# Kernel optimization log

Hardware: AMD Instinct MI355X
Metric: run time of the kernel (lower is better)

## Reference

```python
import jax, jax.numpy as jnp
import numpy as np

N = 16384   # num nodes
E = 524288  # num edges (avg degree 32)
C = 128     # in_channels == hidden_channels (residual requires equality)


def setup_inputs() -> dict:
    key = jax.random.key(0)
    ks = jax.random.split(key, 16)
    s = 1.0 / np.sqrt(C)  # glorot-ish scale
    return {
        "x": jax.random.normal(ks[0], (N, C), dtype=jnp.float32),
        "edge_index": jax.random.randint(ks[1], (2, E), 0, N, dtype=jnp.int32),
        "edge_attr": jax.random.normal(ks[2], (E, 8), dtype=jnp.float32),
        # GATConv 1 params
        "W1": jax.random.normal(ks[3], (C, C), dtype=jnp.float32) * s,
        "a_src1": jax.random.normal(ks[4], (C,), dtype=jnp.float32) * s,
        "a_dst1": jax.random.normal(ks[5], (C,), dtype=jnp.float32) * s,
        "b1": jnp.zeros((C,), dtype=jnp.float32),
        # GATConv 2 params
        "W2": jax.random.normal(ks[6], (C, C), dtype=jnp.float32) * s,
        "a_src2": jax.random.normal(ks[7], (C,), dtype=jnp.float32) * s,
        "a_dst2": jax.random.normal(ks[8], (C,), dtype=jnp.float32) * s,
        "b2": jnp.zeros((C,), dtype=jnp.float32),
        # TemporalAttention params
        "att_weight": jax.random.normal(ks[9], (C, C), dtype=jnp.float32) * s,
        "att_bias": jnp.zeros((C,), dtype=jnp.float32),
        # LayerNorm params
        "ln_gamma": jnp.ones((C,), dtype=jnp.float32),
        "ln_beta": jnp.zeros((C,), dtype=jnp.float32),
    }


def _gat_conv(x, edge_index, W, a_src, a_dst, b):
    """PyG GATConv, heads=1, negative_slope=0.2, add_self_loops=True.
    Edge (j -> i): src = edge_index[0], dst = edge_index[1]; softmax over dst."""
    n = x.shape[0]
    xw = x @ W                                   # [N, C]
    loops = jnp.arange(n, dtype=edge_index.dtype)
    src = jnp.concatenate([edge_index[0], loops])  # [E+N]
    dst = jnp.concatenate([edge_index[1], loops])
    alpha_src = xw @ a_src                       # [N]
    alpha_dst = xw @ a_dst                       # [N]
    e = jax.nn.leaky_relu(alpha_src[src] + alpha_dst[dst], negative_slope=0.2)
    # numerically stable segment softmax over destination nodes
    e_max = jax.ops.segment_max(e, dst, num_segments=n)
    p = jnp.exp(e - e_max[dst])
    denom = jax.ops.segment_sum(p, dst, num_segments=n)
    alpha = p / denom[dst]                       # [E+N]
    out = jax.ops.segment_sum(alpha[:, None] * xw[src], dst, num_segments=n)
    return out + b


def reference(x, edge_index, edge_attr, W1, a_src1, a_dst1, b1,
              W2, a_src2, a_dst2, b2, att_weight, att_bias, ln_gamma, ln_beta):
    # edge_attr is accepted but unused: GATConv was built without edge_dim,
    # so PyG ignores it in the attention computation.
    h = jax.nn.relu(_gat_conv(x, edge_index, W1, a_src1, a_dst1, b1))
    # dropout p=0.2 is identity in eval mode
    h = _gat_conv(h, edge_index, W2, a_src2, a_dst2, b2)

    # TemporalAttention over the (batch=1, N, C) view -> dense NxN attention
    q = h @ att_weight                            # [N, C]
    scores = (q @ h.T) / jnp.sqrt(jnp.float32(h.shape[-1]))  # [N, N]
    attn = jax.nn.softmax(scores, axis=-1)
    h = attn @ h + att_bias                       # [N, C]

    h = h + x                                     # residual
    mu = jnp.mean(h, axis=-1, keepdims=True)
    var = jnp.var(h, axis=-1, keepdims=True)
    h = (h - mu) / jnp.sqrt(var + 1e-5) * ln_gamma + ln_beta
    return h
```

## Files before the change

kernel.cpp:

```cpp
#include <hip/hip_runtime.h>

#define CC 128

typedef __attribute__((ext_vector_type(8))) short bf16x8;
typedef __attribute__((ext_vector_type(16))) float f32x16;

static __device__ __forceinline__ float lrelu(float v){ return v > 0.f ? v : 0.2f*v; }
static __device__ __forceinline__ unsigned short f2bf(float f){
  unsigned u = __float_as_uint(f);
  unsigned r = (u + 0x7fffu + ((u >> 16) & 1u)) >> 16;
  return (unsigned short)r;
}
static __device__ __forceinline__ float bf2f(unsigned short s){
  return __uint_as_float(((unsigned)s) << 16);
}
static __device__ __forceinline__ unsigned cvtpk(float lo, float hi){
  unsigned r;
  asm("v_cvt_pk_bf16_f32 %0, %1, %2" : "=v"(r) : "v"(lo), "v"(hi));
  return r;
}

#define QSCALE (0.08838834764831845f * 1.4426950408889634f)
#define L2E 1.4426950408889634f

#if defined(__has_builtin)
#if __has_builtin(__builtin_amdgcn_global_load_lds)
#define HAVE_GLL 1
#endif
#endif

#ifdef HAVE_GLL
static __device__ __forceinline__ void gload_lds16(const uint4* g, uint4* l){
  __builtin_amdgcn_global_load_lds(
      (const __attribute__((address_space(1))) unsigned int*)(const void*)g,
      (__attribute__((address_space(3))) unsigned int*)(void*)l, 16, 0, 0);
}
#endif

__global__ __launch_bounds__(256) void pack_w3(const float* __restrict__ W1,
                                               const float* __restrict__ W2,
                                               const float* __restrict__ Wa,
                                               unsigned short* __restrict__ img){
  int gid = blockIdx.x*256 + threadIdx.x;
  int m = gid >> 11, u = gid & 2047;
  const float* W = (m==0) ? W1 : (m==1) ? W2 : Wa;
  int k = u >> 8, ct = (u >> 6) & 3, l = u & 63;
  int h = l >> 5, c = ct*32 + (l & 31);
  int k0 = k*16 + h*8;
  float f[8];
  #pragma unroll
  for (int j=0;j<8;j++) f[j] = W[(k0+j)*CC + c];
  uint4 o;
  o.x = cvtpk(f[0],f[1]); o.y = cvtpk(f[2],f[3]);
  o.z = cvtpk(f[4],f[5]); o.w = cvtpk(f[6],f[7]);
  *(uint4*)&img[((size_t)m*2048 + u)*8] = o;
}

template<bool ABF16, int OMODE>
__global__ __launch_bounds__(256) void gemm_mfma(const void* __restrict__ Av,
                                                 const uint4* __restrict__ Wimg,
                                                 unsigned short* __restrict__ out){
  __shared__ uint4 WS[2048];
  const int tid = threadIdx.x, lane = tid & 63, w = tid >> 6;
  const int h = lane >> 5, l31 = lane & 31;
  const long r0 = (long)blockIdx.x * 64;
#ifdef HAVE_GLL
  #pragma unroll
  for (int i=0;i<8;i++){ int u = i*256 + w*64; gload_lds16(Wimg + u + lane, &WS[u]); }
#else
  #pragma unroll
  for (int i=0;i<8;i++){ int u = i*256 + tid; WS[u] = Wimg[u]; }
#endif
  const int rt = w & 1, ct0 = (w >> 1) * 2;
  const long arow = (r0 + rt*32 + l31)*CC + h*8;
  f32x16 acc0 = {}, acc1 = {};
  __syncthreads();
  #pragma unroll
  for (int k=0;k<8;k++){
    bf16x8 afr;
    if (ABF16){
      afr = *(const bf16x8*)&((const unsigned short*)Av)[arow + k*16];
    } else {
      const float* ap = (const float*)Av + arow + k*16;
      float4 a0 = *(const float4*)ap;
      float4 a1 = *(const float4*)(ap+4);
      uint4 av;
      av.x = cvtpk(a0.x,a0.y); av.y = cvtpk(a0.z,a0.w);
      av.z = cvtpk(a1.x,a1.y); av.w = cvtpk(a1.z,a1.w);
      __builtin_memcpy(&afr, &av, 16);
    }
    bf16x8 b0 = *(const bf16x8*)&WS[(k*4+ct0  )*64 + lane];
    bf16x8 b1 = *(const bf16x8*)&WS[(k*4+ct0+1)*64 + lane];
    acc0 = __builtin_amdgcn_mfma_f32_32x32x16_bf16(afr, b0, acc0, 0,0,0);
    acc1 = __builtin_amdgcn_mfma_f32_32x32x16_bf16(afr, b1, acc1, 0,0,0);
  }
  #pragma unroll
  for (int r=0;r<16;r++){
    long row = r0 + rt*32 + (r&3) + 8*(r>>2) + 4*h;
    float s0 = (OMODE==1) ? acc0[r]*QSCALE : acc0[r];
    float s1 = (OMODE==1) ? acc1[r]*QSCALE : acc1[r];
    out[row*CC + ct0*32 + l31]     = f2bf(s0);
    out[row*CC + (ct0+1)*32 + l31] = f2bf(s1);
  }
}

__global__ __launch_bounds__(256) void rowdot2b(const unsigned short* __restrict__ X,
                                                const float* __restrict__ a1,
                                                const float* __restrict__ a2,
                                                float* __restrict__ as_, float* __restrict__ ad_){
  const int lane = threadIdx.x & 63;
  const long row = (long)blockIdx.x*4 + (threadIdx.x >> 6);
  unsigned u = *(const unsigned*)&X[row*CC + lane*2];
  float v0 = bf2f((unsigned short)(u & 0xffffu));
  float v1 = bf2f((unsigned short)(u >> 16));
  float2 w1 = ((const float2*)a1)[lane];
  float2 w2 = ((const float2*)a2)[lane];
  float s1 = v0*w1.x + v1*w1.y;
  float s2 = v0*w2.x + v1*w2.y;
  #pragma unroll
  for (int off=32; off; off>>=1){
    s1 += __shfl_xor(s1, off);
    s2 += __shfl_xor(s2, off);
  }
  if (lane==0){ as_[row]=s1; ad_[row]=s2; }
}

__global__ void zero_int(int* __restrict__ p, int n){
  int i = blockIdx.x*256 + threadIdx.x;
  if (i < n) p[i] = 0;
}
__global__ void csr_hist(const int* __restrict__ ei, int* __restrict__ deg, int E){
  int e = blockIdx.x*256 + threadIdx.x;
  if (e < E) atomicAdd(&deg[ei[E + e]], 1);
}
__global__ __launch_bounds__(256) void csr_scan(const int* __restrict__ deg,
                                                int* __restrict__ rowptr,
                                                int* __restrict__ cursor, int N){
  __shared__ int part[257];
  const int t = threadIdx.x;
  const int per = N / 256;
  const int base = t*per;
  int s = 0;
  for (int j=0;j<per;j++) s += deg[base+j];
  part[t+1] = s;
  if (t==0) part[0] = 0;
  __syncthreads();
  if (t==0){
    for (int i=1;i<=256;i++) part[i] += part[i-1];
  }
  __syncthreads();
  int run = part[t];
  for (int j=0;j<per;j++){
    rowptr[base+j] = run;
    cursor[base+j] = run;
    run += deg[base+j];
  }
  if (t==255) rowptr[N] = run;
}
__global__ void csr_fill(const int* __restrict__ ei, int* __restrict__ cursor,
                         int* __restrict__ csrc, int E){
  int e = blockIdx.x*256 + threadIdx.x;
  if (e < E){
    int d = ei[E + e];
    int slot = atomicAdd(&cursor[d], 1);
    csrc[slot] = ei[e];
  }
}

template<bool RELUOUT>
__global__ __launch_bounds__(256) void gat_gather(
    const int* __restrict__ rowptr, const int* __restrict__ csrc,
    const float* __restrict__ as_, const float* __restrict__ ad_,
    const unsigned short* __restrict__ X, const float* __restrict__ b,
    unsigned short* __restrict__ O, int N){
  const int lane = threadIdx.x & 63;
  const int half = lane >> 5, l32 = lane & 31;
  const int dst = blockIdx.x*4 + (threadIdx.x >> 6);
  const float adv = ad_[dst];
  float m = lrelu(as_[dst] + adv);
  float l = 1.f;
  float acc0=0.f, acc1=0.f, acc2=0.f, acc3=0.f;
  if (half == 0){
    ushort4 v = *(const ushort4*)&X[(size_t)dst*CC + l32*4];
    acc0 = bf2f(v.x); acc1 = bf2f(v.y); acc2 = bf2f(v.z); acc3 = bf2f(v.w);
  }
  const int kb = rowptr[dst];
  const int deg = rowptr[dst+1] - kb;
  for (int c0 = 0; c0 < deg; c0 += 64){
    const int nv = min(64, deg - c0);
    int src = dst; float e = -3.0e38f;
    if (lane < nv){
      src = csrc[kb + c0 + lane];
      e = lrelu(as_[src] + adv);
    }
    float cm = e;
    #pragma unroll
    for (int off=32; off; off>>=1) cm = fmaxf(cm, __shfl_xor(cm, off));
    if (cm > m){
      float fr = __builtin_amdgcn_exp2f((m - cm)*L2E);
      l *= fr; acc0 *= fr; acc1 *= fr; acc2 *= fr; acc3 *= fr;
      m = cm;
    }
    float p = __builtin_amdgcn_exp2f((e - m)*L2E);
    float cs = p;
    #pragma unroll
    for (int off=32; off; off>>=1) cs += __shfl_xor(cs, off);
    l += cs;
    for (int j = 0; j < nv; j += 2){
      float w0 = __shfl(p, j);
      float w1 = __shfl(p, (j+1)&63);
      w1 = (j+1 < nv) ? w1 : 0.f;
      int s0 = __shfl(src, j);
      int s1 = __shfl(src, (j+1)&63);
      float wgt = half ? w1 : w0;
      int s = half ? s1 : s0;
      ushort4 v = *(const ushort4*)&X[(size_t)s*CC + l32*4];
      acc0 += wgt*bf2f(v.x); acc1 += wgt*bf2f(v.y);
      acc2 += wgt*bf2f(v.z); acc3 += wgt*bf2f(v.w);
    }
  }
  acc0 += __shfl_xor(acc0, 32);
  acc1 += __shfl_xor(acc1, 32);
  acc2 += __shfl_xor(acc2, 32);
  acc3 += __shfl_xor(acc3, 32);
  if (half == 0){
    float inv = 1.f / l;
    float4 bb = *(const float4*)&b[l32*4];
    float r0 = acc0*inv + bb.x, r1 = acc1*inv + bb.y;
    float r2 = acc2*inv + bb.z, r3 = acc3*inv + bb.w;
    if (RELUOUT){
      r0=fmaxf(r0,0.f); r1=fmaxf(r1,0.f); r2=fmaxf(r2,0.f); r3=fmaxf(r3,0.f);
    }
    uint2 o; o.x = cvtpk(r0,r1); o.y = cvtpk(r2,r3);
    *(uint2*)&O[(size_t)dst*CC + l32*4] = o;
  }
}

template<int NKT>
__global__ __launch_bounds__(256) void convert_pack(const unsigned short* __restrict__ h,
                                                    uint4* __restrict__ IMG, int N){
  const int KVB = NKT*32;
  int idx = blockIdx.x*256 + threadIdx.x;
  int tile = idx / (NKT*1024);
  int u = idx - tile*(NKT*1024);
  int l = u & 63, hh = l >> 5, l31 = l & 31;
  if (u < NKT*512){
    int kt = u >> 9, ks = (u >> 6) & 7;
    int key = tile*KVB + kt*32 + l31;
    IMG[idx] = *(const uint4*)&h[(size_t)key*CC + ks*16 + hh*8];
  } else {
    int v = u - NKT*512;
    int ks = (v >> 6) & (2*NKT - 1);
    int ct = v >> (NKT==1 ? 7 : 8);
    int c = ct*32 + l31;
    int key0 = tile*KVB + ks*16 + hh*8;
    unsigned short o[8];
    #pragma unroll
    for (int j=0;j<8;j++) o[j] = h[(size_t)(key0+j)*CC + c];
    IMG[idx] = *(uint4*)o;
  }
}

template<int NKT>
__global__ __launch_bounds__(256,2) void attn_mfma(
    const unsigned short* __restrict__ Qb, const uint4* __restrict__ IMG,
    unsigned short* __restrict__ opW, float* __restrict__ ml, int N, int nsplit){
  const int TILE4 = NKT*1024;
  __shared__ uint4 SH[2*NKT*1024];

  const int tid = threadIdx.x;
  const int lane = tid & 63, w = tid >> 6;
  const int h = lane >> 5, q31 = lane & 31;
  const int flat = blockIdx.x;
  const int split = flat % nsplit;
  const int qb0 = (flat / nsplit) * 128;
  const int KVB = NKT*32;
  const int ntt = N / KVB;
  const int tb = (ntt*split)/nsplit, te = (ntt*(split+1))/nsplit;

  bf16x8 qf[8];
  const int qrow = qb0 + w*32 + q31;
  #pragma unroll
  for (int ks=0; ks<8; ks++)
    qf[ks] = *(const bf16x8*)&Qb[(size_t)qrow*CC + ks*16 + h*8];

  f32x16 acc_o[4] = {};
  float m_ = -3.0e38f, l_ = 0.f;

  int cur = 0;
  {
    const uint4* src = IMG + (size_t)tb*TILE4;
#ifdef HAVE_GLL
    #pragma unroll
    for (int i=0;i<NKT*4;i++){ int u = i*256 + w*64; gload_lds16(src + u + lane, &SH[u]); }
#else
    #pragma unroll
    for (int i=0;i<NKT*4;i++){ int u = i*256 + tid; SH[u] = src[u]; }
#endif
  }

  for (int t=tb; t<te; t++){
    __syncthreads();
    if (t+1 < te){
      const uint4* src = IMG + (size_t)(t+1)*TILE4;
      uint4* dst = &SH[(cur^1)*TILE4];
#ifdef HAVE_GLL
      #pragma unroll
      for (int i=0;i<NKT*4;i++){ int u = i*256 + w*64; gload_lds16(src + u + lane, dst + u); }
#else
      #pragma unroll
      for (int i=0;i<NKT*4;i++){ int u = i*256 + tid; dst[u] = src[u]; }
#endif
    }
    const uint4* B = &SH[cur*TILE4];

    f32x16 accs[NKT];
    #pragma unroll
    for (int kt=0; kt<NKT; kt++){
      f32x16 a = {};
      __builtin_amdgcn_s_setprio(1);
      #pragma unroll
      for (int ks=0; ks<8; ks++){
        bf16x8 hf = *(const bf16x8*)&B[(kt*8+ks)*64 + lane];
        a = __builtin_amdgcn_mfma_f32_32x32x16_bf16(hf, qf[ks], a, 0,0,0);
      }
      __builtin_amdgcn_s_setprio(0);
      accs[kt] = a;
    }

    float tmax[16];
    #pragma unroll
    for (int r=0;r<16;r++){
      float v = accs[0][r];
      if (NKT == 2) v = fmaxf(v, accs[1][r]);
      tmax[r] = v;
    }
    #pragma unroll
    for (int s=8; s; s>>=1)
      #pragma unroll
      for (int r=0;r<s;r++) tmax[r] = fmaxf(tmax[r], tmax[r+s]);
    float tm = fmaxf(tmax[0], __shfl_xor(tmax[0], 32));
    if (!__all(tm <= m_ + 11.0f)){
      float mn = fmaxf(m_, tm);
      float fr = __builtin_amdgcn_exp2f(m_ - mn);
      m_ = mn; l_ *= fr;
      #pragma unroll
      for (int ct=0; ct<4; ct++)
        #pragma unroll
        for (int r=0;r<16;r++) acc_o[ct][r] *= fr;
    }
    float psum[16];
    #pragma unroll
    for (int kt=0; kt<NKT; kt++)
      #pragma unroll
      for (int r=0;r<16;r++)
        accs[kt][r] = __builtin_amdgcn_exp2f(accs[kt][r] - m_);
    #pragma unroll
    for (int r=0;r<16;r++){
      float v = accs[0][r];
      if (NKT == 2) v += accs[1][r];
      psum[r] = v;
    }
    #pragma unroll
    for (int s=8; s; s>>=1)
      #pragma unroll
      for (int r=0;r<s;r++) psum[r] += psum[r+s];
    l_ += psum[0] + __shfl_xor(psum[0], 32);

    unsigned pk[NKT][8];
    #pragma unroll
    for (int kt=0; kt<NKT; kt++)
      #pragma unroll
      for (int wd=0; wd<8; wd++)
        pk[kt][wd] = cvtpk(accs[kt][2*wd], accs[kt][2*wd+1]);

    #pragma unroll
    for (int ks=0; ks<2*NKT; ks++){
      const int kt = ks >> 1, W = (ks & 1)*4;
      unsigned w0o = pk[kt][W+0], w1o = pk[kt][W+1];
      unsigned w2o = pk[kt][W+2], w3o = pk[kt][W+3];
      unsigned va = h ? w0o : w2o;
      unsigned vb = h ? w1o : w3o;
      unsigned fa = (unsigned)__shfl_xor((int)va, 32);
      unsigned fb = (unsigned)__shfl_xor((int)vb, 32);
      uint4 fw;
      fw.x = h ? fa : w0o;
      fw.y = h ? fb : w1o;
      fw.z = h ? w2o : fa;
      fw.w = h ? w3o : fb;
      bf16x8 pfrag;
      __builtin_memcpy(&pfrag, &fw, 16);
      __builtin_amdgcn_s_setprio(1);
      #pragma unroll
      for (int ct=0; ct<4; ct++){
        bf16x8 hf = *(const bf16x8*)&B[NKT*512 + (ct*2*NKT+ks)*64 + lane];
        acc_o[ct] = __builtin_amdgcn_mfma_f32_32x32x16_bf16(hf, pfrag, acc_o[ct], 0,0,0);
      }
      __builtin_amdgcn_s_setprio(0);
    }
    cur ^= 1;
  }

  float inv = 1.f / l_;
  unsigned apk[4][8];
  #pragma unroll
  for (int ct=0; ct<4; ct++)
    #pragma unroll
    for (int wd=0; wd<8; wd++)
      apk[ct][wd] = cvtpk(acc_o[ct][2*wd]*inv, acc_o[ct][2*wd+1]*inv);

  unsigned short* orow = opW + (size_t)split*N*CC + (size_t)qrow*CC + h*64;
  #pragma unroll
  for (int cp=0; cp<2; cp++){
    #pragma unroll
    for (int jp=0; jp<4; jp++){
      int wd0 = 2*jp, wd1 = 2*jp+1;
      unsigned a0 = apk[cp][wd0],   a1 = apk[cp][wd1];
      unsigned b0 = apk[cp+2][wd0], b1 = apk[cp+2][wd1];
      unsigned v0 = h ? a0 : b0;
      unsigned v1 = h ? a1 : b1;
      unsigned f0 = (unsigned)__shfl_xor((int)v0, 32);
      unsigned f1 = (unsigned)__shfl_xor((int)v1, 32);
      unsigned o0 = h ? b0 : a0;
      unsigned o1 = h ? b1 : a1;
      uint4 st;
      st.x = h ? f0 : o0;
      st.y = h ? f1 : o1;
      st.z = h ? o0 : f0;
      st.w = h ? o1 : f1;
      *(uint4*)&orow[cp*32 + jp*8] = st;
    }
  }
  if (lane < 32)
    ((float2*)ml)[(size_t)split*N + qrow] = make_float2(m_, l_);
}

template<int NS>
__global__ __launch_bounds__(256) void merge_ln(
    const unsigned short* __restrict__ opW, const float* __restrict__ ml,
    const float* __restrict__ x, const float* __restrict__ ab,
    const float* __restrict__ gam, const float* __restrict__ bet,
    float* __restrict__ out, int N){
  const int lane = threadIdx.x & 63;
  const long row = (long)blockIdx.x*4 + (threadIdx.x >> 6);
  float mm[NS], ll[NS];
  float M = -3.0e38f;
  #pragma unroll
  for (int i=0;i<NS;i++){
    float2 v = ((const float2*)ml)[(size_t)i*N + row];
    mm[i]=v.x; ll[i]=v.y;
    M = fmaxf(M, v.x);
  }
  float den = 0.f;
  float wgt[NS];
  #pragma unroll
  for (int i=0;i<NS;i++){ wgt[i] = exp2f(mm[i]-M)*ll[i]; den += wgt[i]; }
  float invd = 1.f/den;
  float o0 = 0.f, o1 = 0.f;
  #pragma unroll
  for (int i=0;i<NS;i++){
    unsigned u = *(const unsigned*)&opW[((size_t)i*N + row)*CC + lane*2];
    float c = wgt[i]*invd;
    o0 += c * bf2f((unsigned short)(u & 0xffffu));
    o1 += c * bf2f((unsigned short)(u >> 16));
  }
  float2 xb = ((const float2*)(x + row*CC))[lane];
  float2 bb = ((const float2*)ab)[lane];
  float a0 = o0 + bb.x + xb.x;
  float a1 = o1 + bb.y + xb.y;
  float s = a0 + a1, ss = a0*a0 + a1*a1;
  #pragma unroll
  for (int off=32; off; off>>=1){ s += __shfl_xor(s,off); ss += __shfl_xor(ss,off); }
  float mu  = s * (1.f/128.f);
  float var = ss * (1.f/128.f) - mu*mu;
  float rstd = rsqrtf(var + 1e-5f);
  float2 gg = ((const float2*)gam)[lane];
  float2 b2 = ((const float2*)bet)[lane];
  float2 r;
  r.x = (a0 - mu)*rstd*gg.x + b2.x;
  r.y = (a1 - mu)*rstd*gg.y + b2.y;
  ((float2*)(out + row*CC))[lane] = r;
}

extern "C" void kernel_launch(void* const* d_in, const int* in_sizes, int n_in,
                              void* d_out, int out_size, void* d_ws, size_t ws_size,
                              hipStream_t stream) {
  const float* x   = (const float*)d_in[0];
  const int*   ei  = (const int*)d_in[1];
  const float* W1  = (const float*)d_in[3];
  const float* a_s1= (const float*)d_in[4];
  const float* a_d1= (const float*)d_in[5];
  const float* b1  = (const float*)d_in[6];
  const float* W2  = (const float*)d_in[7];
  const float* a_s2= (const float*)d_in[8];
  const float* a_d2= (const float*)d_in[9];
  const float* b2  = (const float*)d_in[10];
  const float* Wa  = (const float*)d_in[11];
  const float* ab  = (const float*)d_in[12];
  const float* g   = (const float*)d_in[13];
  const float* be  = (const float*)d_in[14];
  float* out = (float*)d_out;

  const int N = in_sizes[0] / CC;
  const int E = in_sizes[1] / 2;
  const size_t MB = 1024*1024;
  const size_t KB = 1024;

  char* base = (char*)d_ws;
  uint4* IMG  = (uint4*)(base);
  unsigned short* xwb = (unsigned short*)(base + 8*MB);
  unsigned short* hW  = (unsigned short*)(base + 12*MB);
  int* csrc   = (int*)(base + 16*MB);
  int* rowptr = (int*)(base + 18*MB);
  int* cursor = (int*)(base + 18*MB + 128*KB);
  int* deg    = (int*)(base + 18*MB + 256*KB);
  float* as_  = (float*)(base + 18*MB + 384*KB);
  float* ad_  = (float*)(base + 18*MB + 512*KB);
  unsigned short* Wimg = (unsigned short*)(base + 19*MB);
  unsigned short* opW  = (unsigned short*)(base + 8*MB);
  unsigned short* QbD  = (unsigned short*)d_out;

  const uint4* W1i = (const uint4*)(Wimg);
  const uint4* W2i = (const uint4*)(Wimg + 2048*8);
  const uint4* Wai = (const uint4*)(Wimg + 2*2048*8);

  const bool big = (ws_size >= 41*MB);
  const int ns = big ? 8 : 4;
  float* ml = (float*)(base + 8*MB + (size_t)ns*4*MB);

  dim3 B(256);

  pack_w3<<<24, B, 0, stream>>>(W1, W2, Wa, Wimg);
  zero_int<<<(N+255)/256, B, 0, stream>>>(deg, N);
  csr_hist<<<(E+255)/256, B, 0, stream>>>(ei, deg, E);
  csr_scan<<<1, B, 0, stream>>>(deg, rowptr, cursor, N);
  csr_fill<<<(E+255)/256, B, 0, stream>>>(ei, cursor, csrc, E);

  gemm_mfma<false,0><<<N/64, B, 0, stream>>>(x, W1i, xwb);
  rowdot2b<<<N/4, B, 0, stream>>>(xwb, a_s1, a_d1, as_, ad_);
  gat_gather<true><<<N/4, B, 0, stream>>>(rowptr, csrc, as_, ad_, xwb, b1, hW, N);

  gemm_mfma<true,0><<<N/64, B, 0, stream>>>(hW, W2i, xwb);
  rowdot2b<<<N/4, B, 0, stream>>>(xwb, a_s2, a_d2, as_, ad_);
  gat_gather<false><<<N/4, B, 0, stream>>>(rowptr, csrc, as_, ad_, xwb, b2, hW, N);

  gemm_mfma<true,1><<<N/64, B, 0, stream>>>(hW, Wai, QbD);
  if (big){
    convert_pack<1><<<(N*32)/256, B, 0, stream>>>(hW, IMG, N);
    attn_mfma<1><<<(N/128)*8, B, 0, stream>>>(QbD, IMG, opW, ml, N, 8);
    merge_ln<8><<<N/4, B, 0, stream>>>(opW, ml, x, ab, g, be, out, N);
  } else {
    convert_pack<2><<<(N*32)/256, B, 0, stream>>>(hW, IMG, N);
    attn_mfma<2><<<(N/128)*4, B, 0, stream>>>(QbD, IMG, opW, ml, N, 4);
    merge_ln<4><<<N/4, B, 0, stream>>>(opW, ml, x, ab, g, be, out, N);
  }
}
```

Before: 332.5 us.

## Process two query tiles per wave in attention kernel to reuse K/V fragments

Each wave in the flash-attention kernel now handles NQT query tiles of 32 rows. Every K/V fragment loaded from LDS feeds NQT MFMAs instead of one. The big path uses NQT=2 with half as many blocks, so LDS traffic and tile loads per query drop. The cost is doubled accumulator and Q-fragment registers, which may cause spills or lower occupancy under launch_bounds(256,2), and fewer blocks are available to fill the GPU.

After: 321.0 us. 3.4% less time.

```diff
diff --git a/kernel.cpp b/kernel.cpp
--- a/kernel.cpp
+++ b/kernel.cpp
@@ -261,7 +261,7 @@
   }
 }
 
-template<int NKT>
+template<int NKT, int NQT>
 __global__ __launch_bounds__(256,2) void attn_mfma(
     const unsigned short* __restrict__ Qb, const uint4* __restrict__ IMG,
     unsigned short* __restrict__ opW, float* __restrict__ ml, int N, int nsplit){
@@ -273,19 +273,30 @@
   const int h = lane >> 5, q31 = lane & 31;
   const int flat = blockIdx.x;
   const int split = flat % nsplit;
-  const int qb0 = (flat / nsplit) * 128;
+  const int qb0 = (flat / nsplit) * (128*NQT);
   const int KVB = NKT*32;
   const int ntt = N / KVB;
   const int tb = (ntt*split)/nsplit, te = (ntt*(split+1))/nsplit;
 
-  bf16x8 qf[8];
-  const int qrow = qb0 + w*32 + q31;
-  #pragma unroll
-  for (int ks=0; ks<8; ks++)
-    qf[ks] = *(const bf16x8*)&Qb[(size_t)qrow*CC + ks*16 + h*8];
-
-  f32x16 acc_o[4] = {};
-  float m_ = -3.0e38f, l_ = 0.f;
+  int qrow[NQT];
+  bf16x8 qf[NQT][8];
+  #pragma unroll
+  for (int qt=0; qt<NQT; qt++){
+    qrow[qt] = qb0 + w*(32*NQT) + qt*32 + q31;
+    #pragma unroll
+    for (int ks=0; ks<8; ks++)
+      qf[qt][ks] = *(const bf16x8*)&Qb[(size_t)qrow[qt]*CC + ks*16 + h*8];
+  }
+
+  f32x16 zero16 = {};
+  f32x16 acc_o[4][NQT];
+  #pragma unroll
+  for (int ct=0; ct<4; ct++)
+    #pragma unroll
+    for (int qt=0; qt<NQT; qt++) acc_o[ct][qt] = zero16;
+  float m_[NQT], l_[NQT];
+  #pragma unroll
+  for (int qt=0; qt<NQT; qt++){ m_[qt] = -3.0e38f; l_[qt] = 0.f; }
 
   int cur = 0;
   {
@@ -314,125 +325,147 @@
     }
     const uint4* B = &SH[cur*TILE4];
 
-    f32x16 accs[NKT];
+    f32x16 accs[NKT][NQT];
     #pragma unroll
     for (int kt=0; kt<NKT; kt++){
-      f32x16 a = {};
+      #pragma unroll
+      for (int qt=0; qt<NQT; qt++) accs[kt][qt] = zero16;
       __builtin_amdgcn_s_setprio(1);
       #pragma unroll
       for (int ks=0; ks<8; ks++){
         bf16x8 hf = *(const bf16x8*)&B[(kt*8+ks)*64 + lane];
-        a = __builtin_amdgcn_mfma_f32_32x32x16_bf16(hf, qf[ks], a, 0,0,0);
+        #pragma unroll
+        for (int qt=0; qt<NQT; qt++)
+          accs[kt][qt] = __builtin_amdgcn_mfma_f32_32x32x16_bf16(hf, qf[qt][ks], accs[kt][qt], 0,0,0);
       }
       __builtin_amdgcn_s_setprio(0);
-      accs[kt] = a;
-    }
-
-    float tmax[16];
-    #pragma unroll
-    for (int r=0;r<16;r++){
-      float v = accs[0][r];
-      if (NKT == 2) v = fmaxf(v, accs[1][r]);
-      tmax[r] = v;
-    }
-    #pragma unroll
-    for (int s=8; s; s>>=1)
-      #pragma unroll
-      for (int r=0;r<s;r++) tmax[r] = fmaxf(tmax[r], tmax[r+s]);
-    float tm = fmaxf(tmax[0], __shfl_xor(tmax[0], 32));
-    if (!__all(tm <= m_ + 11.0f)){
-      float mn = fmaxf(m_, tm);
-      float fr = __builtin_amdgcn_exp2f(m_ - mn);
-      m_ = mn; l_ *= fr;
-      #pragma unroll
-      for (int ct=0; ct<4; ct++)
-        #pragma unroll
-        for (int r=0;r<16;r++) acc_o[ct][r] *= fr;
-    }
-    float psum[16];
-    #pragma unroll
-    for (int kt=0; kt<NKT; kt++)
-      #pragma unroll
-      for (int r=0;r<16;r++)
-        accs[kt][r] = __builtin_amdgcn_exp2f(accs[kt][r] - m_);
-    #pragma unroll
-    for (int r=0;r<16;r++){
-      float v = accs[0][r];
-      if (NKT == 2) v += accs[1][r];
-      psum[r] = v;
-    }
-    #pragma unroll
-    for (int s=8; s; s>>=1)
-      #pragma unroll
-      for (int r=0;r<s;r++) psum[r] += psum[r+s];
-    l_ += psum[0] + __shfl_xor(psum[0], 32);
-
-    unsigned pk[NKT][8];
-    #pragma unroll
-    for (int kt=0; kt<NKT; kt++)
-      #pragma unroll
-      for (int wd=0; wd<8; wd++)
-        pk[kt][wd] = cvtpk(accs[kt][2*wd], accs[kt][2*wd+1]);
+    }
+
+    float tm[NQT];
+    #pragma unroll
+    for (int qt=0; qt<NQT; qt++){
+      float tmax[16];
+      #pragma unroll
+      for (int r=0;r<16;r++){
+        float v = accs[0][qt][r];
+        if (NKT == 2) v = fmaxf(v, accs[1][qt][r]);
+        tmax[r] = v;
+      }
+      #pragma unroll
+      for (int s=8; s; s>>=1)
+        #pragma unroll
+        for (int r=0;r<s;r++) tmax[r] = fmaxf(tmax[r], tmax[r+s]);
+      tm[qt] = fmaxf(tmax[0], __shfl_xor(tmax[0], 32));
+    }
+    bool ok = true;
+    #pragma unroll
+    for (int qt=0; qt<NQT; qt++) ok &= (tm[qt] <= m_[qt] + 11.0f);
+    if (!__all(ok)){
+      #pragma unroll
+      for (int qt=0; qt<NQT; qt++){
+        float mn = fmaxf(m_[qt], tm[qt]);
+        float fr = __builtin_amdgcn_exp2f(m_[qt] - mn);
+        m_[qt] = mn; l_[qt] *= fr;
+        #pragma unroll
+        for (int ct=0; ct<4; ct++)
+          #pragma unroll
+          for (int r=0;r<16;r++) acc_o[ct][qt][r] *= fr;
+      }
+    }
+    unsigned pk[NQT][NKT][8];
+    #pragma unroll
+    for (int qt=0; qt<NQT; qt++){
+      float psum[16];
+      #pragma unroll
+      for (int kt=0; kt<NKT; kt++)
+        #pragma unroll
+        for (int r=0;r<16;r++)
+          accs[kt][qt][r] = __builtin_amdgcn_exp2f(accs[kt][qt][r] - m_[qt]);
+      #pragma unroll
+      for (int r=0;r<16;r++){
+        float v = accs[0][qt][r];
+        if (NKT == 2) v += accs[1][qt][r];
+        psum[r] = v;
+      }
+      #pragma unroll
+      for (int s=8; s; s>>=1)
+        #pragma unroll
+        for (int r=0;r<s;r++) psum[r] += psum[r+s];
+      l_[qt] += psum[0] + __shfl_xor(psum[0], 32);
+      #pragma unroll
+      for (int kt=0; kt<NKT; kt++)
+        #pragma unroll
+        for (int wd=0; wd<8; wd++)
+          pk[qt][kt][wd] = cvtpk(accs[kt][qt][2*wd], accs[kt][qt][2*wd+1]);
+    }
 
     #pragma unroll
     for (int ks=0; ks<2*NKT; ks++){
       const int kt = ks >> 1, W = (ks & 1)*4;
-      unsigned w0o = pk[kt][W+0], w1o = pk[kt][W+1];
-      unsigned w2o = pk[kt][W+2], w3o = pk[kt][W+3];
-      unsigned va = h ? w0o : w2o;
-      unsigned vb = h ? w1o : w3o;
-      unsigned fa = (unsigned)__shfl_xor((int)va, 32);
-      unsigned fb = (unsigned)__shfl_xor((int)vb, 32);
-      uint4 fw;
-      fw.x = h ? fa : w0o;
-      fw.y = h ? fb : w1o;
-      fw.z = h ? w2o : fa;
-      fw.w = h ? w3o : fb;
-      bf16x8 pfrag;
-      __builtin_memcpy(&pfrag, &fw, 16);
+      bf16x8 pfrag[NQT];
+      #pragma unroll
+      for (int qt=0; qt<NQT; qt++){
+        unsigned w0o = pk[qt][kt][W+0], w1o = pk[qt][kt][W+1];
+        unsigned w2o = pk[qt][kt][W+2], w3o = pk[qt][kt][W+3];
+        unsigned va = h ? w0o : w2o;
+        unsigned vb = h ? w1o : w3o;
+        unsigned fa = (unsigned)__shfl_xor((int)va, 32);
+        unsigned fb = (unsigned)__shfl_xor((int)vb, 32);
+        uint4 fw;
+        fw.x = h ? fa : w0o;
+        fw.y = h ? fb : w1o;
+        fw.z = h ? w2o : fa;
+        fw.w = h ? w3o : fb;
+        __builtin_memcpy(&pfrag[qt], &fw, 16);
+      }
       __builtin_amdgcn_s_setprio(1);
       #pragma unroll
       for (int ct=0; ct<4; ct++){
         bf16x8 hf = *(const bf16x8*)&B[NKT*512 + (ct*2*NKT+ks)*64 + lane];
-        acc_o[ct] = __builtin_amdgcn_mfma_f32_32x32x16_bf16(hf, pfrag, acc_o[ct], 0,0,0);
+        #pragma unroll
+        for (int qt=0; qt<NQT; qt++)
+          acc_o[ct][qt] = __builtin_amdgcn_mfma_f32_32x32x16_bf16(hf, pfrag[qt], acc_o[ct][qt], 0,0,0);
       }
       __builtin_amdgcn_s_setprio(0);
     }
     cur ^= 1;
   }
 
-  float inv = 1.f / l_;
-  unsigned apk[4][8];
-  #pragma unroll
-  for (int ct=0; ct<4; ct++)
-    #pragma unroll
-    for (int wd=0; wd<8; wd++)
-      apk[ct][wd] = cvtpk(acc_o[ct][2*wd]*inv, acc_o[ct][2*wd+1]*inv);
-
-  unsigned short* orow = opW + (size_t)split*N*CC + (size_t)qrow*CC + h*64;
-  #pragma unroll
-  for (int cp=0; cp<2; cp++){
-    #pragma unroll
-    for (int jp=0; jp<4; jp++){
-      int wd0 = 2*jp, wd1 = 2*jp+1;
-      unsigned a0 = apk[cp][wd0],   a1 = apk[cp][wd1];
-      unsigned b0 = apk[cp+2][wd0], b1 = apk[cp+2][wd1];
-      unsigned v0 = h ? a0 : b0;
-      unsigned v1 = h ? a1 : b1;
-      unsigned f0 = (unsigned)__shfl_xor((int)v0, 32);
-      unsigned f1 = (unsigned)__shfl_xor((int)v1, 32);
-      unsigned o0 = h ? b0 : a0;
-      unsigned o1 = h ? b1 : a1;
-      uint4 st;
-      st.x = h ? f0 : o0;
-      st.y = h ? f1 : o1;
-      st.z = h ? o0 : f0;
-      st.w = h ? o1 : f1;
-      *(uint4*)&orow[cp*32 + jp*8] = st;
-    }
-  }
-  if (lane < 32)
-    ((float2*)ml)[(size_t)split*N + qrow] = make_float2(m_, l_);
+  #pragma unroll
+  for (int qt=0; qt<NQT; qt++){
+    float inv = 1.f / l_[qt];
+    unsigned apk[4][8];
+    #pragma unroll
+    for (int ct=0; ct<4; ct++)
+      #pragma unroll
+      for (int wd=0; wd<8; wd++)
+        apk[ct][wd] = cvtpk(acc_o[ct][qt][2*wd]*inv, acc_o[ct][qt][2*wd+1]*inv);
+
+    unsigned short* orow = opW + (size_t)split*N*CC + (size_t)qrow[qt]*CC + h*64;
+    #pragma unroll
+    for (int cp=0; cp<2; cp++){
+      #pragma unroll
+      for (int jp=0; jp<4; jp++){
+        int wd0 = 2*jp, wd1 = 2*jp+1;
+        unsigned a0 = apk[cp][wd0],   a1 = apk[cp][wd1];
+        unsigned b0 = apk[cp+2][wd0], b1 = apk[cp+2][wd1];
+        unsigned v0 = h ? a0 : b0;
+        unsigned v1 = h ? a1 : b1;
+        unsigned f0 = (unsigned)__shfl_xor((int)v0, 32);
+        unsigned f1 = (unsigned)__shfl_xor((int)v1, 32);
+        unsigned o0 = h ? b0 : a0;
+        unsigned o1 = h ? b1 : a1;
+        uint4 st;
+        st.x = h ? f0 : o0;
+        st.y = h ? f1 : o1;
+        st.z = h ? o0 : f0;
+        st.w = h ? o1 : f1;
+        *(uint4*)&orow[cp*32 + jp*8] = st;
+      }
+    }
+    if (lane < 32)
+      ((float2*)ml)[(size_t)split*N + qrow[qt]] = make_float2(m_[qt], l_[qt]);
+  }
 }
 
 template<int NS>
@@ -547,11 +580,11 @@
   gemm_mfma<true,1><<<N/64, B, 0, stream>>>(hW, Wai, QbD);
   if (big){
     convert_pack<1><<<(N*32)/256, B, 0, stream>>>(hW, IMG, N);
-    attn_mfma<1><<<(N/128)*8, B, 0, stream>>>(QbD, IMG, opW, ml, N, 8);
+    attn_mfma<1,2><<<(N/256)*8, B, 0, stream>>>(QbD, IMG, opW, ml, N, 8);
     merge_ln<8><<<N/4, B, 0, stream>>>(opW, ml, x, ab, g, be, out, N);
   } else {
     convert_pack<2><<<(N*32)/256, B, 0, stream>>>(hW, IMG, N);
-    attn_mfma<2><<<(N/128)*4, B, 0, stream>>>(QbD, IMG, opW, ml, N, 4);
+    attn_mfma<2,1><<<(N/128)*4, B, 0, stream>>>(QbD, IMG, opW, ml, N, 4);
     merge_ln<4><<<N/4, B, 0, stream>>>(opW, ml, x, ab, g, be, out, N);
   }
 }
```

## Software-pipeline flash attention with triple-buffered tiles overlapping QK and PV

Applied to the files above, without the earlier changes.

Replaces the double-buffered attention kernel with one that stages 32-key tiles into three LDS buffers. It issues the QK^T MFMAs for the next tile while the current tile's softmax and PV product run. The aim is to hide the softmax's exp/reduction latency and the tile loads behind matrix-core work. The tile size is fixed at 32 keys for all sizes, and the loop is unrolled by two, which assumes an even tile count per split. Register pressure rises because two score tiles are live at once, and the setprio hints are dropped.

Result: no change. 336.1 us (+1.1%).

```diff
diff --git a/kernel.cpp b/kernel.cpp
--- a/kernel.cpp
+++ b/kernel.cpp
@@ -236,24 +236,22 @@
   }
 }
 
-template<int NKT>
 __global__ __launch_bounds__(256) void convert_pack(const unsigned short* __restrict__ h,
                                                     uint4* __restrict__ IMG, int N){
-  const int KVB = NKT*32;
   int idx = blockIdx.x*256 + threadIdx.x;
-  int tile = idx / (NKT*1024);
-  int u = idx - tile*(NKT*1024);
+  int tile = idx >> 10;
+  int u = idx & 1023;
   int l = u & 63, hh = l >> 5, l31 = l & 31;
-  if (u < NKT*512){
-    int kt = u >> 9, ks = (u >> 6) & 7;
-    int key = tile*KVB + kt*32 + l31;
+  if (u < 512){
+    int ks = u >> 6;
+    int key = tile*32 + l31;
     IMG[idx] = *(const uint4*)&h[(size_t)key*CC + ks*16 + hh*8];
   } else {
-    int v = u - NKT*512;
-    int ks = (v >> 6) & (2*NKT - 1);
-    int ct = v >> (NKT==1 ? 7 : 8);
+    int v = u - 512;
+    int ks = (v >> 6) & 1;
+    int ct = v >> 7;
     int c = ct*32 + l31;
-    int key0 = tile*KVB + ks*16 + hh*8;
+    int key0 = tile*32 + ks*16 + hh*8;
     unsigned short o[8];
     #pragma unroll
     for (int j=0;j<8;j++) o[j] = h[(size_t)(key0+j)*CC + c];
@@ -261,12 +259,89 @@
   }
 }
 
-template<int NKT>
-__global__ __launch_bounds__(256,2) void attn_mfma(
+static __device__ __forceinline__ void stage_tile(uint4* dst, const uint4* src, int w, int lane){
+#ifdef HAVE_GLL
+  #pragma unroll
+  for (int i=0;i<4;i++) gload_lds16(src + i*256 + w*64 + lane, dst + i*256 + w*64);
+#else
+  int tid = w*64 + lane;
+  #pragma unroll
+  for (int i=0;i<4;i++) dst[i*256 + tid] = src[i*256 + tid];
+#endif
+}
+
+static __device__ __forceinline__ f32x16 sphase(const uint4* buf, const bf16x8 (&qf)[8], int lane){
+  f32x16 a = {};
+  #pragma unroll
+  for (int ks=0; ks<8; ks++){
+    bf16x8 hf = *(const bf16x8*)&buf[ks*64 + lane];
+    a = __builtin_amdgcn_mfma_f32_32x32x16_bf16(hf, qf[ks], a, 0,0,0);
+  }
+  return a;
+}
+
+static __device__ __forceinline__ void softmax_pk(f32x16& s, float& m_, float& l_,
+                                                  f32x16 (&acc_o)[4], unsigned (&pk)[8]){
+  float tmax[16];
+  #pragma unroll
+  for (int r=0;r<16;r++) tmax[r] = s[r];
+  #pragma unroll
+  for (int st=8; st; st>>=1)
+    #pragma unroll
+    for (int r=0;r<st;r++) tmax[r] = fmaxf(tmax[r], tmax[r+st]);
+  float tm = fmaxf(tmax[0], __shfl_xor(tmax[0], 32));
+  if (!__all(tm <= m_ + 11.0f)){
+    float mn = fmaxf(m_, tm);
+    float fr = __builtin_amdgcn_exp2f(m_ - mn);
+    m_ = mn; l_ *= fr;
+    #pragma unroll
+    for (int ct=0; ct<4; ct++)
+      #pragma unroll
+      for (int r=0;r<16;r++) acc_o[ct][r] *= fr;
+  }
+  #pragma unroll
+  for (int r=0;r<16;r++) s[r] = __builtin_amdgcn_exp2f(s[r] - m_);
+  float ps[16];
+  #pragma unroll
+  for (int r=0;r<16;r++) ps[r] = s[r];
+  #pragma unroll
+  for (int st=8; st; st>>=1)
+    #pragma unroll
+    for (int r=0;r<st;r++) ps[r] += ps[r+st];
+  l_ += ps[0] + __shfl_xor(ps[0], 32);
+  #pragma unroll
+  for (int wd=0; wd<8; wd++) pk[wd] = cvtpk(s[2*wd], s[2*wd+1]);
+}
+
+static __device__ __forceinline__ void pvphase(const uint4* buf, const unsigned (&pk)[8],
+                                               f32x16 (&acc_o)[4], int lane, int h){
+  #pragma unroll
+  for (int ks=0; ks<2; ks++){
+    const int W = ks*4;
+    unsigned w0o = pk[W+0], w1o = pk[W+1], w2o = pk[W+2], w3o = pk[W+3];
+    unsigned va = h ? w0o : w2o;
+    unsigned vb = h ? w1o : w3o;
+    unsigned fa = (unsigned)__shfl_xor((int)va, 32);
+    unsigned fb = (unsigned)__shfl_xor((int)vb, 32);
+    uint4 fw;
+    fw.x = h ? fa : w0o;
+    fw.y = h ? fb : w1o;
+    fw.z = h ? w2o : fa;
+    fw.w = h ? w3o : fb;
+    bf16x8 pfrag;
+    __builtin_memcpy(&pfrag, &fw, 16);
+    #pragma unroll
+    for (int ct=0; ct<4; ct++){
+      bf16x8 hf = *(const bf16x8*)&buf[512 + (ct*2+ks)*64 + lane];
+      acc_o[ct] = __builtin_amdgcn_mfma_f32_32x32x16_bf16(hf, pfrag, acc_o[ct], 0,0,0);
+    }
+  }
+}
+
+__global__ __launch_bounds__(256,2) void attn_pipe(
     const unsigned short* __restrict__ Qb, const uint4* __restrict__ IMG,
     unsigned short* __restrict__ opW, float* __restrict__ ml, int N, int nsplit){
-  const int TILE4 = NKT*1024;
-  __shared__ uint4 SH[2*NKT*1024];
+  __shared__ uint4 SH[3*1024];
 
   const int tid = threadIdx.x;
   const int lane = tid & 63, w = tid >> 6;
@@ -274,8 +349,7 @@
   const int flat = blockIdx.x;
   const int split = flat % nsplit;
   const int qb0 = (flat / nsplit) * 128;
-  const int KVB = NKT*32;
-  const int ntt = N / KVB;
+  const int ntt = N >> 5;
   const int tb = (ntt*split)/nsplit, te = (ntt*(split+1))/nsplit;
 
   bf16x8 qf[8];
@@ -287,118 +361,37 @@
   f32x16 acc_o[4] = {};
   float m_ = -3.0e38f, l_ = 0.f;
 
-  int cur = 0;
-  {
-    const uint4* src = IMG + (size_t)tb*TILE4;
-#ifdef HAVE_GLL
-    #pragma unroll
-    for (int i=0;i<NKT*4;i++){ int u = i*256 + w*64; gload_lds16(src + u + lane, &SH[u]); }
-#else
-    #pragma unroll
-    for (int i=0;i<NKT*4;i++){ int u = i*256 + tid; SH[u] = src[u]; }
-#endif
-  }
-
-  for (int t=tb; t<te; t++){
-    __syncthreads();
-    if (t+1 < te){
-      const uint4* src = IMG + (size_t)(t+1)*TILE4;
-      uint4* dst = &SH[(cur^1)*TILE4];
-#ifdef HAVE_GLL
-      #pragma unroll
-      for (int i=0;i<NKT*4;i++){ int u = i*256 + w*64; gload_lds16(src + u + lane, dst + u); }
-#else
-      #pragma unroll
-      for (int i=0;i<NKT*4;i++){ int u = i*256 + tid; dst[u] = src[u]; }
-#endif
-    }
-    const uint4* B = &SH[cur*TILE4];
-
-    f32x16 accs[NKT];
-    #pragma unroll
-    for (int kt=0; kt<NKT; kt++){
-      f32x16 a = {};
-      __builtin_amdgcn_s_setprio(1);
-      #pragma unroll
-      for (int ks=0; ks<8; ks++){
-        bf16x8 hf = *(const bf16x8*)&B[(kt*8+ks)*64 + lane];
-        a = __builtin_amdgcn_mfma_f32_32x32x16_bf16(hf, qf[ks], a, 0,0,0);
-      }
-      __builtin_amdgcn_s_setprio(0);
-      accs[kt] = a;
-    }
-
-    float tmax[16];
-    #pragma unroll
-    for (int r=0;r<16;r++){
-      float v = accs[0][r];
-      if (NKT == 2) v = fmaxf(v, accs[1][r]);
-      tmax[r] = v;
-    }
-    #pragma unroll
-    for (int s=8; s; s>>=1)
-      #pragma unroll
-      for (int r=0;r<s;r++) tmax[r] = fmaxf(tmax[r], tmax[r+s]);
-    float tm = fmaxf(tmax[0], __shfl_xor(tmax[0], 32));
-    if (!__all(tm <= m_ + 11.0f)){
-      float mn = fmaxf(m_, tm);
-      float fr = __builtin_amdgcn_exp2f(m_ - mn);
-      m_ = mn; l_ *= fr;
-      #pragma unroll
-      for (int ct=0; ct<4; ct++)
-        #pragma unroll
-        for (int r=0;r<16;r++) acc_o[ct][r] *= fr;
-    }
-    float psum[16];
-    #pragma unroll
-    for (int kt=0; kt<NKT; kt++)
-      #pragma unroll
-      for (int r=0;r<16;r++)
-        accs[kt][r] = __builtin_amdgcn_exp2f(accs[kt][r] - m_);
-    #pragma unroll
-    for (int r=0;r<16;r++){
-      float v = accs[0][r];
-      if (NKT == 2) v += accs[1][r];
-      psum[r] = v;
-    }
-    #pragma unroll
-    for (int s=8; s; s>>=1)
-      #pragma unroll
-      for (int r=0;r<s;r++) psum[r] += psum[r+s];
-    l_ += psum[0] + __shfl_xor(psum[0], 32);
-
-    unsigned pk[NKT][8];
-    #pragma unroll
-    for (int kt=0; kt<NKT; kt++)
-      #pragma unroll
-      for (int wd=0; wd<8; wd++)
-        pk[kt][wd] = cvtpk(accs[kt][2*wd], accs[kt][2*wd+1]);
-
-    #pragma unroll
-    for (int ks=0; ks<2*NKT; ks++){
-      const int kt = ks >> 1, W = (ks & 1)*4;
-      unsigned w0o = pk[kt][W+0], w1o = pk[kt][W+1];
-      unsigned w2o = pk[kt][W+2], w3o = pk[kt][W+3];
-      unsigned va = h ? w0o : w2o;
-      unsigned vb = h ? w1o : w3o;
-      unsigned fa = (unsigned)__shfl_xor((int)va, 32);
-      unsigned fb = (unsigned)__shfl_xor((int)vb, 32);
-      uint4 fw;
-      fw.x = h ? fa : w0o;
-      fw.y = h ? fb : w1o;
-      fw.z = h ? w2o : fa;
-      fw.w = h ? w3o : fb;
-      bf16x8 pfrag;
-      __builtin_memcpy(&pfrag, &fw, 16);
-      __builtin_amdgcn_s_setprio(1);
-      #pragma unroll
-      for (int ct=0; ct<4; ct++){
-        bf16x8 hf = *(const bf16x8*)&B[NKT*512 + (ct*2*NKT+ks)*64 + lane];
-        acc_o[ct] = __builtin_amdgcn_mfma_f32_32x32x16_bf16(hf, pfrag, acc_o[ct], 0,0,0);
-      }
-      __builtin_amdgcn_s_setprio(0);
-    }
-    cur ^= 1;
+  uint4* pc = SH;
+  uint4* pn = SH + 1024;
+  uint4* ps = SH + 2048;
+
+  stage_tile(pc, IMG + (size_t)tb*1024, w, lane);
+  __syncthreads();
+  if (tb+1 < te) stage_tile(pn, IMG + (size_t)(tb+1)*1024, w, lane);
+  f32x16 sA = sphase(pc, qf, lane);
+  f32x16 sB;
+  __syncthreads();
+  if (tb+2 < te) stage_tile(ps, IMG + (size_t)(tb+2)*1024, w, lane);
+
+  for (int t = tb; t < te; t += 2){
+    {
+      unsigned pk[8];
+      softmax_pk(sA, m_, l_, acc_o, pk);
+      sB = sphase(pn, qf, lane);
+      pvphase(pc, pk, acc_o, lane, h);
+      __syncthreads();
+      if (t+3 < te) stage_tile(pc, IMG + (size_t)(t+3)*1024, w, lane);
+      uint4* tmp = pc; pc = pn; pn = ps; ps = tmp;
+    }
+    {
+      unsigned pk[8];
+      softmax_pk(sB, m_, l_, acc_o, pk);
+      if (t+2 < te) sA = sphase(pn, qf, lane);
+      pvphase(pc, pk, acc_o, lane, h);
+      __syncthreads();
+      if (t+4 < te) stage_tile(pc, IMG + (size_t)(t+4)*1024, w, lane);
+      uint4* tmp = pc; pc = pn; pn = ps; ps = tmp;
+    }
   }
 
   float inv = 1.f / l_;
@@ -545,13 +538,11 @@
   gat_gather<false><<<N/4, B, 0, stream>>>(rowptr, csrc, as_, ad_, xwb, b2, hW, N);
 
   gemm_mfma<true,1><<<N/64, B, 0, stream>>>(hW, Wai, QbD);
-  if (big){
-    convert_pack<1><<<(N*32)/256, B, 0, stream>>>(hW, IMG, N);
-    attn_mfma<1><<<(N/128)*8, B, 0, stream>>>(QbD, IMG, opW, ml, N, 8);
+  convert_pack<<<(N*32)/256, B, 0, stream>>>(hW, IMG, N);
+  attn_pipe<<<(N/128)*ns, B, 0, stream>>>(QbD, IMG, opW, ml, N, ns);
+
+  if (big)
     merge_ln<8><<<N/4, B, 0, stream>>>(opW, ml, x, ab, g, be, out, N);
-  } else {
-    convert_pack<2><<<(N*32)/256, B, 0, stream>>>(hW, IMG, N);
-    attn_mfma<2><<<(N/128)*4, B, 0, stream>>>(QbD, IMG, opW, ml, N, 4);
+  else
     merge_ln<4><<<N/4, B, 0, stream>>>(opW, ml, x, ab, g, be, out, N);
-  }
-}
+}
```
